# Optimization experiments

Measured on AMD Instinct MI355X. Metric: run time of the kernel, lower is better.

## Reference

```python
import jax, jax.numpy as jnp
import numpy as np

HEADS = 16
LN_EPS = 1e-12
MINUS_INF = -10000.0  # matches DeepSpeed's minus_inf constant


def setup_inputs() -> dict:
    key = jax.random.key(0)
    ks = jax.random.split(key, 6)
    B, S, H = 2, 2048, 2048
    x = jax.random.normal(ks[0], (B, S, H), dtype=jnp.float32)
    mask = jnp.zeros((B, 1, 1, S), dtype=jnp.float32)  # additive float mask (no padding)
    qkvw = jax.random.normal(ks[1], (H, 3 * H), dtype=jnp.float32) * 0.02
    qkvb = jax.random.normal(ks[2], (3 * H,), dtype=jnp.float32) * 0.02
    ow = jax.random.normal(ks[3], (H, H), dtype=jnp.float32) * 0.02
    norm_w = jnp.ones((H,), dtype=jnp.float32)
    norm_b = jnp.zeros((H,), dtype=jnp.float32)
    return {"x": x, "mask": mask, "qkvw": qkvw, "qkvb": qkvb, "ow": ow,
            "norm_w": norm_w, "norm_b": norm_b}


def _layernorm(x, g, b):
    mu = jnp.mean(x, axis=-1, keepdims=True)
    var = jnp.mean(jnp.square(x - mu), axis=-1, keepdims=True)
    return (x - mu) * jax.lax.rsqrt(var + LN_EPS) * g + b


def reference(x, mask, qkvw, qkvb, ow, norm_w, norm_b):
    B, S, H = x.shape
    dh = H // HEADS
    # QKVGemmOp: fused layernorm + QKV projection
    inp_norm = _layernorm(x, norm_w, norm_b)                      # [B,S,H]
    qkv = jnp.einsum('bsh,he->bse', inp_norm, qkvw) + qkvb        # [B,S,3H]
    q, k, v = jnp.split(qkv, 3, axis=-1)
    q = q.reshape(B, S, HEADS, dh).transpose(0, 2, 1, 3)          # [B,Hd,S,dh]
    k = k.reshape(B, S, HEADS, dh).transpose(0, 2, 1, 3)
    v = v.reshape(B, S, HEADS, dh).transpose(0, 2, 1, 3)
    # SoftmaxContextOp: kernel scales q and k each by 1/norm_factor,
    # norm_factor = d_head**0.25 (use_mup=False) -> net scale 1/sqrt(d_head)
    scale = 1.0 / jnp.sqrt(jnp.asarray(dh, dtype=x.dtype))
    scores = jnp.einsum('bhqd,bhkd->bhqk', q, k) * scale          # [B,Hd,S,S]
    causal = jnp.tril(jnp.ones((S, S), dtype=bool))
    scores = jnp.where(causal[None, None], scores + mask, MINUS_INF)
    probs = jax.nn.softmax(scores, axis=-1)
    ctx = jnp.einsum('bhqk,bhkd->bhqd', probs, v)                 # [B,Hd,S,dh]
    ctx = ctx.transpose(0, 2, 1, 3).reshape(B, S, H)
    # VectorMatMulOp: output projection (no bias here)
    out = jnp.einsum('bsh,ho->bso', ctx, ow)                      # [B,S,H]
    return (out, k, v, ctx, inp_norm)
```

## Files before the change

kernel.cpp:

```cpp
#include <hip/hip_runtime.h>

typedef short bf16x8 __attribute__((ext_vector_type(8)));
typedef float floatx4 __attribute__((ext_vector_type(4)));

#define MFMA16(a, b, c) __builtin_amdgcn_mfma_f32_16x16x32_bf16((a), (b), (c), 0, 0, 0)

__device__ __forceinline__ unsigned short f2bf(float f) {
    union { float f; unsigned int u; } v; v.f = f;
    unsigned int u = v.u;
    return (unsigned short)((u + 0x7FFFu + ((u >> 16) & 1u)) >> 16);
}

__device__ __forceinline__ void gld_lds16(const void* g, void* l) {
    __builtin_amdgcn_global_load_lds(
        (const __attribute__((address_space(1))) unsigned int*)g,
        (__attribute__((address_space(3))) unsigned int*)l, 16, 0, 0);
}

__global__ __launch_bounds__(256) void ln_kernel(
        const float* __restrict__ x, const float* __restrict__ g,
        const float* __restrict__ be, float* __restrict__ yo,
        unsigned short* __restrict__ yb) {
    int row = blockIdx.x, t = threadIdx.x;
    const float* xr = x + (size_t)row * 2048;
    float4 a = ((const float4*)xr)[2 * t];
    float4 b = ((const float4*)xr)[2 * t + 1];
    float s = a.x + a.y + a.z + a.w + b.x + b.y + b.z + b.w;
    float q = a.x * a.x + a.y * a.y + a.z * a.z + a.w * a.w +
              b.x * b.x + b.y * b.y + b.z * b.z + b.w * b.w;
    for (int m = 1; m < 64; m <<= 1) { s += __shfl_xor(s, m); q += __shfl_xor(q, m); }
    __shared__ float red[8];
    if ((t & 63) == 0) { red[t >> 6] = s; red[4 + (t >> 6)] = q; }
    __syncthreads();
    s = red[0] + red[1] + red[2] + red[3];
    q = red[4] + red[5] + red[6] + red[7];
    float mean = s * (1.0f / 2048.0f);
    float var = q * (1.0f / 2048.0f) - mean * mean;
    float rs = rsqrtf(var + 1e-12f);
    float4 g0 = ((const float4*)g)[2 * t], g1 = ((const float4*)g)[2 * t + 1];
    float4 b0 = ((const float4*)be)[2 * t], b1 = ((const float4*)be)[2 * t + 1];
    float4 y0, y1;
    y0.x = (a.x - mean) * rs * g0.x + b0.x;
    y0.y = (a.y - mean) * rs * g0.y + b0.y;
    y0.z = (a.z - mean) * rs * g0.z + b0.z;
    y0.w = (a.w - mean) * rs * g0.w + b0.w;
    y1.x = (b.x - mean) * rs * g1.x + b1.x;
    y1.y = (b.y - mean) * rs * g1.y + b1.y;
    y1.z = (b.z - mean) * rs * g1.z + b1.z;
    y1.w = (b.w - mean) * rs * g1.w + b1.w;
    float* yr = yo + (size_t)row * 2048;
    ((float4*)yr)[2 * t] = y0;
    ((float4*)yr)[2 * t + 1] = y1;
    union { unsigned short u[8]; uint4 v; } pk;
    pk.u[0] = f2bf(y0.x); pk.u[1] = f2bf(y0.y); pk.u[2] = f2bf(y0.z); pk.u[3] = f2bf(y0.w);
    pk.u[4] = f2bf(y1.x); pk.u[5] = f2bf(y1.y); pk.u[6] = f2bf(y1.z); pk.u[7] = f2bf(y1.w);
    *(uint4*)(yb + (size_t)row * 2048 + t * 8) = pk.v;
}

__global__ __launch_bounds__(256) void transpose_cvt(
        const float* __restrict__ src, unsigned short* __restrict__ dst,
        int K, int N) {
    __shared__ unsigned short tile[64][73];
    int n0 = blockIdx.x * 64, k0 = blockIdx.y * 64;
    size_t bo = (size_t)blockIdx.z * K * N;
    int t = threadIdx.x;
    for (int p = 0; p < 4; p++) {
        int idx = p * 256 + t; int r = idx >> 4; int c = (idx & 15) * 4;
        float4 v = *(const float4*)(src + bo + (size_t)(k0 + r) * N + n0 + c);
        tile[r][c] = f2bf(v.x); tile[r][c + 1] = f2bf(v.y);
        tile[r][c + 2] = f2bf(v.z); tile[r][c + 3] = f2bf(v.w);
    }
    __syncthreads();
    for (int p = 0; p < 4; p++) {
        int idx = p * 256 + t; int n = idx >> 4; int c = (idx & 15) * 4;
        ushort4 o;
        o.x = tile[c][n]; o.y = tile[c + 1][n];
        o.z = tile[c + 2][n]; o.w = tile[c + 3][n];
        *(ushort4*)(dst + bo + (size_t)(n0 + n) * K + k0 + c) = o;
    }
}

#define NT_QKV 32

__device__ __forceinline__ void stage_A(const unsigned short* __restrict__ Ag,
        unsigned short* As, int mh, int m0, int kt, int tid) {
#pragma unroll
    for (int j = 0; j < 2; j++) {
        int G = j * 512 + tid;
        int s = (G >> 3) & 63;
        int gr = G & 7;
        int row = j * 128 + mh * 64 + s;
        const unsigned short* src =
            Ag + (size_t)(m0 + row) * 2048 + kt * 64 + ((gr ^ (s & 7)) << 3);
        unsigned short* dst = As + j * 8192 + mh * 4096 + (tid >> 6) * 512;
        gld_lds16(src, dst);
    }
}

__device__ __forceinline__ void stage_B(const unsigned short* __restrict__ Bg,
        unsigned short* Bs, int nh, int n0, int kt, int tid) {
#pragma unroll
    for (int j = 0; j < 2; j++) {
        int G = j * 512 + tid;
        int wcc = G >> 8;
        int s = (G >> 3) & 31;
        int gr = G & 7;
        int row = wcc * 64 + nh * 32 + s;
        const unsigned short* src =
            Bg + (size_t)(n0 + row) * 2048 + kt * 64 + ((gr ^ (s & 7)) << 3);
        unsigned short* dst = Bs + wcc * 4096 + nh * 2048 + ((tid >> 6) & 3) * 512;
        gld_lds16(src, dst);
    }
}

__device__ __forceinline__ bf16x8 ldfrag(const unsigned short* S, int row, int ks,
                                         int quad, int ln15) {
    int gr = ((ks << 2) | quad) ^ (ln15 & 7);
    return *(const bf16x8*)(S + row * 64 + gr * 8);
}

__device__ __forceinline__ void qkv_tile(
        const unsigned short* __restrict__ Ag, const unsigned short* __restrict__ Bg,
        unsigned short* Asc, unsigned short* Bsc,
        unsigned short* Asn, unsigned short* Bsn,
        int t, int m0, int n0, int tid, int wr, int wc, int ln15, int quad,
        floatx4 (&acc)[8][4]) {
    bf16x8 a[4][2], bb[2][2];
#pragma unroll
    for (int m = 0; m < 4; m++) {
        a[m][0] = ldfrag(Asc, wr * 128 + m * 16 + ln15, 0, quad, ln15);
        a[m][1] = ldfrag(Asc, wr * 128 + m * 16 + ln15, 1, quad, ln15);
    }
#pragma unroll
    for (int n = 0; n < 2; n++) {
        bb[n][0] = ldfrag(Bsc, wc * 64 + n * 16 + ln15, 0, quad, ln15);
        bb[n][1] = ldfrag(Bsc, wc * 64 + n * 16 + ln15, 1, quad, ln15);
    }
    if (t + 1 < NT_QKV) stage_B(Bg, Bsn, 0, n0, t + 1, tid);
    __builtin_amdgcn_s_barrier();
    asm volatile("s_waitcnt lgkmcnt(0)" ::: "memory");
    __builtin_amdgcn_sched_barrier(0);
    __builtin_amdgcn_s_setprio(1);
#pragma unroll
    for (int m = 0; m < 4; m++)
#pragma unroll
        for (int n = 0; n < 2; n++) {
            acc[m][n] = MFMA16(a[m][0], bb[n][0], acc[m][n]);
            acc[m][n] = MFMA16(a[m][1], bb[n][1], acc[m][n]);
        }
    __builtin_amdgcn_s_setprio(0);
    __builtin_amdgcn_s_barrier();
#pragma unroll
    for (int n = 0; n < 2; n++) {
        bb[n][0] = ldfrag(Bsc, wc * 64 + (2 + n) * 16 + ln15, 0, quad, ln15);
        bb[n][1] = ldfrag(Bsc, wc * 64 + (2 + n) * 16 + ln15, 1, quad, ln15);
    }
    if (t + 2 < NT_QKV) stage_A(Ag, Asc, 0, m0, t + 2, tid);
    __builtin_amdgcn_s_barrier();
    asm volatile("s_waitcnt lgkmcnt(0)" ::: "memory");
    __builtin_amdgcn_sched_barrier(0);
    __builtin_amdgcn_s_setprio(1);
#pragma unroll
    for (int m = 0; m < 4; m++)
#pragma unroll
        for (int n = 0; n < 2; n++) {
            acc[m][2 + n] = MFMA16(a[m][0], bb[n][0], acc[m][2 + n]);
            acc[m][2 + n] = MFMA16(a[m][1], bb[n][1], acc[m][2 + n]);
        }
    __builtin_amdgcn_s_setprio(0);
    __builtin_amdgcn_s_barrier();
#pragma unroll
    for (int m = 0; m < 4; m++) {
        a[m][0] = ldfrag(Asc, wr * 128 + (4 + m) * 16 + ln15, 0, quad, ln15);
        a[m][1] = ldfrag(Asc, wr * 128 + (4 + m) * 16 + ln15, 1, quad, ln15);
    }
    if (t + 2 < NT_QKV) stage_B(Bg, Bsc, 1, n0, t + 2, tid);
    __builtin_amdgcn_s_barrier();
    asm volatile("s_waitcnt lgkmcnt(0)" ::: "memory");
    __builtin_amdgcn_sched_barrier(0);
    __builtin_amdgcn_s_setprio(1);
#pragma unroll
    for (int m = 0; m < 4; m++)
#pragma unroll
        for (int n = 0; n < 2; n++) {
            acc[4 + m][2 + n] = MFMA16(a[m][0], bb[n][0], acc[4 + m][2 + n]);
            acc[4 + m][2 + n] = MFMA16(a[m][1], bb[n][1], acc[4 + m][2 + n]);
        }
    __builtin_amdgcn_s_setprio(0);
    __builtin_amdgcn_s_barrier();
#pragma unroll
    for (int n = 0; n < 2; n++) {
        bb[n][0] = ldfrag(Bsc, wc * 64 + n * 16 + ln15, 0, quad, ln15);
        bb[n][1] = ldfrag(Bsc, wc * 64 + n * 16 + ln15, 1, quad, ln15);
    }
    if (t + 2 < NT_QKV) stage_A(Ag, Asc, 1, m0, t + 2, tid);
    __builtin_amdgcn_s_barrier();
    asm volatile("s_waitcnt lgkmcnt(0)" ::: "memory");
    __builtin_amdgcn_sched_barrier(0);
    __builtin_amdgcn_s_setprio(1);
#pragma unroll
    for (int m = 0; m < 4; m++)
#pragma unroll
        for (int n = 0; n < 2; n++) {
            acc[4 + m][n] = MFMA16(a[m][0], bb[n][0], acc[4 + m][n]);
            acc[4 + m][n] = MFMA16(a[m][1], bb[n][1], acc[4 + m][n]);
        }
    __builtin_amdgcn_s_setprio(0);
    if (t + 2 < NT_QKV) asm volatile("s_waitcnt vmcnt(6)" ::: "memory");
    else                asm volatile("s_waitcnt vmcnt(0)" ::: "memory");
    __builtin_amdgcn_s_barrier();
}

__global__ __launch_bounds__(512, 2) void gemm_qkv(
        const unsigned short* __restrict__ A, const unsigned short* __restrict__ Bt,
        const float* __restrict__ bias, float* __restrict__ ko,
        float* __restrict__ vo, unsigned short* __restrict__ qws,
        unsigned short* __restrict__ kbf) {
    __shared__ __align__(16) unsigned short As[2][16384];
    __shared__ __align__(16) unsigned short Bs[2][16384];
    int bid = blockIdx.x;
    int wg = (bid & 7) * 48 + (bid >> 3);
    int mt = wg / 24, ntile = wg % 24;
    int m0 = mt * 256, n0 = ntile * 256;
    int tid = threadIdx.x;
    int wave = tid >> 6, lane = tid & 63, ln15 = lane & 15, quad = lane >> 4;
    int wr = wave >> 2, wc = wave & 3;
    floatx4 acc[8][4] = {};
    stage_B(Bt, Bs[0], 0, n0, 0, tid);
    stage_A(A, As[0], 0, m0, 0, tid);
    stage_B(Bt, Bs[0], 1, n0, 0, tid);
    stage_A(A, As[0], 1, m0, 0, tid);
    stage_A(A, As[1], 0, m0, 1, tid);
    stage_B(Bt, Bs[1], 1, n0, 1, tid);
    stage_A(A, As[1], 1, m0, 1, tid);
    asm volatile("s_waitcnt vmcnt(6)" ::: "memory");
    __builtin_amdgcn_s_barrier();
#pragma unroll 1
    for (int t = 0; t < NT_QKV; t += 2) {
        qkv_tile(A, Bt, As[0], Bs[0], As[1], Bs[1], t,     m0, n0, tid, wr, wc, ln15, quad, acc);
        qkv_tile(A, Bt, As[1], Bs[1], As[0], Bs[0], t + 1, m0, n0, tid, wr, wc, ln15, quad, acc);
    }
#pragma unroll
    for (int mi = 0; mi < 8; mi++) {
        int row = m0 + wr * 128 + mi * 16 + quad * 4;
#pragma unroll
        for (int ni = 0; ni < 4; ni++) {
            int col = n0 + wc * 64 + ni * 16 + ln15;
            float bv = bias[col];
#pragma unroll
            for (int r = 0; r < 4; r++) {
                float val = acc[mi][ni][r] + bv;
                int rr = row + r;
                int b = rr >> 11, s = rr & 2047;
                if (col < 2048) {
                    qws[(size_t)rr * 2048 + col] = f2bf(val);
                } else if (col < 4096) {
                    int cc = col - 2048; int h = cc >> 7, d = cc & 127;
                    size_t o = ((size_t)(b * 16 + h) * 2048 + s) * 128 + d;
                    ko[o] = val;
                    kbf[o] = f2bf(val);
                } else {
                    int cc = col - 4096; int h = cc >> 7, d = cc & 127;
                    vo[((size_t)(b * 16 + h) * 2048 + s) * 128 + d] = val;
                }
            }
        }
    }
}

__global__ __launch_bounds__(256) void gemm_out(
        const float* __restrict__ Actx, const unsigned short* __restrict__ Bt,
        float* __restrict__ out) {
    __shared__ unsigned short As[128 * 72];
    __shared__ unsigned short Bs[128 * 72];
    int m0 = blockIdx.y * 128, n0 = blockIdx.x * 128;
    int t = threadIdx.x;
    int wave = t >> 6, lane = t & 63, ln15 = lane & 15, quad = lane >> 4;
    int wm = wave >> 1, wn = wave & 1;
    floatx4 acc[4][4] = {};
    for (int k0 = 0; k0 < 2048; k0 += 64) {
        for (int p = 0; p < 4; p++) {
            int idx = p * 256 + t; int r = idx >> 3; int c = (idx & 7) * 8;
            const float* ap = Actx + (size_t)(m0 + r) * 2048 + k0 + c;
            float4 u0 = ((const float4*)ap)[0], u1 = ((const float4*)ap)[1];
            union { unsigned short u[8]; uint4 v; } pk;
            pk.u[0] = f2bf(u0.x); pk.u[1] = f2bf(u0.y); pk.u[2] = f2bf(u0.z); pk.u[3] = f2bf(u0.w);
            pk.u[4] = f2bf(u1.x); pk.u[5] = f2bf(u1.y); pk.u[6] = f2bf(u1.z); pk.u[7] = f2bf(u1.w);
            *(uint4*)&As[r * 72 + c] = pk.v;
            *(uint4*)&Bs[r * 72 + c] = *(const uint4*)(Bt + (size_t)(n0 + r) * 2048 + k0 + c);
        }
        __syncthreads();
        for (int ks = 0; ks < 2; ks++) {
            bf16x8 af[4], bfr[4];
            for (int i = 0; i < 4; i++)
                af[i] = *(const bf16x8*)&As[(wm * 64 + i * 16 + ln15) * 72 + ks * 32 + quad * 8];
            for (int i = 0; i < 4; i++)
                bfr[i] = *(const bf16x8*)&Bs[(wn * 64 + i * 16 + ln15) * 72 + ks * 32 + quad * 8];
            for (int mi = 0; mi < 4; mi++)
                for (int ni = 0; ni < 4; ni++)
                    acc[mi][ni] = MFMA16(af[mi], bfr[ni], acc[mi][ni]);
        }
        __syncthreads();
    }
    for (int mi = 0; mi < 4; mi++) {
        int row = m0 + wm * 64 + mi * 16 + quad * 4;
        for (int ni = 0; ni < 4; ni++) {
            int col = n0 + wn * 64 + ni * 16 + ln15;
            for (int r = 0; r < 4; r++)
                out[(size_t)(row + r) * 2048 + col] = acc[mi][ni][r];
        }
    }
}

__global__ __launch_bounds__(256) void attn_kernel(
        const unsigned short* __restrict__ qws, const unsigned short* __restrict__ kbf,
        const unsigned short* __restrict__ vT, const float* __restrict__ mask,
        float* __restrict__ ctxo) {
    __shared__ unsigned short Ks[64 * 136];
    __shared__ unsigned short Vt[128 * 72];
    __shared__ unsigned short Pl[4 * 16 * 72];
    int jp = blockIdx.x, h = blockIdx.y, b = blockIdx.z;
    int t = threadIdx.x, wave = t >> 6, lane = t & 63, ln15 = lane & 15, quad = lane >> 4;
    const float scale = 0.08838834764831845f;

    const unsigned short* kb = kbf + (size_t)(b * 16 + h) * 2048 * 128;
    const unsigned short* vTb = vT + (size_t)(b * 16 + h) * 128 * 2048;
    const float* mb = mask + (size_t)b * 2048;

    for (int half = 0; half < 2; half++) {
        int qt = half ? (31 - jp) : jp;
        int Q0 = qt * 64;

        bf16x8 qf[4];
        const unsigned short* qbase =
            qws + ((size_t)(b * 2048 + Q0 + wave * 16 + ln15)) * 2048 + h * 128;
        for (int ks = 0; ks < 4; ks++)
            qf[ks] = *(const bf16x8*)(qbase + ks * 32 + quad * 8);

        float m_r[4], l_r[4];
        floatx4 o[8] = {};
        for (int r = 0; r < 4; r++) { m_r[r] = -1e30f; l_r[r] = 0.0f; }

        int nkt = qt + 1;
        for (int kt = 0; kt < nkt; kt++) {
            int c0 = kt * 64;
            for (int p = 0; p < 4; p++) {
                int idx = p * 256 + t; int r = idx >> 4; int c = (idx & 15) * 8;
                *(uint4*)&Ks[r * 136 + c] = *(const uint4*)(kb + (size_t)(c0 + r) * 128 + c);
            }
            for (int p = 0; p < 4; p++) {
                int idx = p * 256 + t; int d = idx >> 3; int sg = (idx & 7) * 8;
                *(uint4*)&Vt[d * 72 + sg] = *(const uint4*)(vTb + (size_t)d * 2048 + c0 + sg);
            }
            __syncthreads();

            floatx4 cs[4] = {};
            for (int ks = 0; ks < 4; ks++)
                for (int ni = 0; ni < 4; ni++) {
                    bf16x8 kfr = *(const bf16x8*)&Ks[(ni * 16 + ln15) * 136 + ks * 32 + quad * 8];
                    cs[ni] = MFMA16(qf[ks], kfr, cs[ni]);
                }

            float sv[4][4];
            float mt[4] = {-1e30f, -1e30f, -1e30f, -1e30f};
            if (kt == qt) {
                for (int ni = 0; ni < 4; ni++) {
                    int cg = c0 + ni * 16 + ln15;
                    float mk = mb[cg];
                    for (int r = 0; r < 4; r++) {
                        int qg = Q0 + wave * 16 + quad * 4 + r;
                        float v = (cg <= qg) ? cs[ni][r] * scale + mk : -10000.0f;
                        sv[ni][r] = v;
                        mt[r] = fmaxf(mt[r], v);
                    }
                }
            } else {
                for (int ni = 0; ni < 4; ni++) {
                    float mk = mb[c0 + ni * 16 + ln15];
                    for (int r = 0; r < 4; r++) {
                        float v = cs[ni][r] * scale + mk;
                        sv[ni][r] = v;
                        mt[r] = fmaxf(mt[r], v);
                    }
                }
            }
            for (int m = 1; m < 16; m <<= 1)
                for (int r = 0; r < 4; r++) mt[r] = fmaxf(mt[r], __shfl_xor(mt[r], m));
            float alpha[4], lt[4];
            for (int r = 0; r < 4; r++) {
                float mn = fmaxf(m_r[r], mt[r]);
                alpha[r] = __expf(m_r[r] - mn);
                m_r[r] = mn;
                lt[r] = 0.0f;
            }
            for (int ni = 0; ni < 4; ni++)
                for (int r = 0; r < 4; r++) {
                    float p = __expf(sv[ni][r] - m_r[r]);
                    sv[ni][r] = p;
                    lt[r] += p;
                }
            for (int m = 1; m < 16; m <<= 1)
                for (int r = 0; r < 4; r++) lt[r] += __shfl_xor(lt[r], m);
            for (int r = 0; r < 4; r++) l_r[r] = l_r[r] * alpha[r] + lt[r];
            for (int nj = 0; nj < 8; nj++)
                for (int r = 0; r < 4; r++) o[nj][r] *= alpha[r];

            unsigned short* pw = &Pl[wave * 16 * 72];
            for (int ni = 0; ni < 4; ni++)
                for (int r = 0; r < 4; r++)
                    pw[(quad * 4 + r) * 72 + ni * 16 + ln15] = f2bf(sv[ni][r]);

            for (int ks2 = 0; ks2 < 2; ks2++) {
                bf16x8 pf = *(const bf16x8*)&Pl[(wave * 16 + ln15) * 72 + ks2 * 32 + quad * 8];
                for (int nj = 0; nj < 8; nj++) {
                    bf16x8 vf = *(const bf16x8*)&Vt[(nj * 16 + ln15) * 72 + ks2 * 32 + quad * 8];
                    o[nj] = MFMA16(pf, vf, o[nj]);
                }
            }
            __syncthreads();
        }

        float rl[4];
        for (int r = 0; r < 4; r++) rl[r] = 1.0f / l_r[r];
        for (int nj = 0; nj < 8; nj++)
            for (int r = 0; r < 4; r++) {
                int s = Q0 + wave * 16 + quad * 4 + r;
                ctxo[((size_t)(b * 2048 + s)) * 2048 + h * 128 + nj * 16 + ln15] = o[nj][r] * rl[r];
            }
    }
}

extern "C" void kernel_launch(void* const* d_in, const int* in_sizes, int n_in,
                              void* d_out, int out_size, void* d_ws, size_t ws_size,
                              hipStream_t stream) {
    const float* x      = (const float*)d_in[0];
    const float* mask   = (const float*)d_in[1];
    const float* qkvw   = (const float*)d_in[2];
    const float* qkvb   = (const float*)d_in[3];
    const float* ow     = (const float*)d_in[4];
    const float* norm_w = (const float*)d_in[5];
    const float* norm_b = (const float*)d_in[6];

    float* out      = (float*)d_out;
    float* k_out    = out + 8388608;
    float* v_out    = out + 16777216;
    float* ctx_out  = out + 25165824;
    float* norm_out = out + 33554432;

    unsigned short* ws    = (unsigned short*)d_ws;
    unsigned short* xn    = ws;
    unsigned short* qkvwT = ws + 8388608;
    unsigned short* owT   = ws + 8388608 + 12582912;
    unsigned short* qws   = owT + 4194304;
    unsigned short* vT    = qws + 8388608;
    unsigned short* kbf   = vT + 8388608;

    ln_kernel<<<4096, 256, 0, stream>>>(x, norm_w, norm_b, norm_out, xn);
    transpose_cvt<<<dim3(96, 32, 1), 256, 0, stream>>>(qkvw, qkvwT, 2048, 6144);
    transpose_cvt<<<dim3(32, 32, 1), 256, 0, stream>>>(ow, owT, 2048, 2048);
    gemm_qkv<<<dim3(384), 512, 0, stream>>>(xn, qkvwT, qkvb, k_out, v_out, qws, kbf);
    transpose_cvt<<<dim3(2, 32, 32), 256, 0, stream>>>(v_out, vT, 2048, 128);
    attn_kernel<<<dim3(16, 16, 2), 256, 0, stream>>>(qws, kbf, vT, mask, ctx_out);
    gemm_out<<<dim3(16, 32), 256, 0, stream>>>(ctx_out, owT, out);
}
```

Before: 543.9 us.

## Restructure QKV GEMM prefetch to one-tile double buffering and remap tiles per XCD

The QKV GEMM prologue now stages only the first K-tile. Inside the loop, each phase prefetches the next tile's A and B halves into the alternate LDS buffer, instead of loading two tiles ahead into the current buffer. Every phase now ends with a uniform vmcnt(4) wait plus barrier, wrapped in new sync macros. The block-to-tile mapping is also changed so each XCD works on a contiguous 4x12 region of M×N tiles, aiming for better L2 reuse of A and B. The shallower prefetch depth and the extra vmcnt waits per phase may expose more global-load latency.

```diff
diff --git a/kernel.cpp b/kernel.cpp
--- a/kernel.cpp
+++ b/kernel.cpp
@@ -119,6 +119,17 @@
     return *(const bf16x8*)(S + row * 64 + gr * 8);
 }
 
+#define PHASE_SYNC()                                        \
+    __builtin_amdgcn_s_barrier();                           \
+    asm volatile("s_waitcnt lgkmcnt(0)" ::: "memory");      \
+    __builtin_amdgcn_sched_barrier(0);                      \
+    __builtin_amdgcn_s_setprio(1)
+
+#define PHASE_END()                                         \
+    __builtin_amdgcn_s_setprio(0);                          \
+    asm volatile("s_waitcnt vmcnt(4)" ::: "memory");        \
+    __builtin_amdgcn_s_barrier()
+
 __device__ __forceinline__ void qkv_tile(
         const unsigned short* __restrict__ Ag, const unsigned short* __restrict__ Bg,
         unsigned short* Asc, unsigned short* Bsc,
@@ -126,6 +137,7 @@
         int t, int m0, int n0, int tid, int wr, int wc, int ln15, int quad,
         floatx4 (&acc)[8][4]) {
     bf16x8 a[4][2], bb[2][2];
+    bool pf = (t + 1 < NT_QKV);
 #pragma unroll
     for (int m = 0; m < 4; m++) {
         a[m][0] = ldfrag(Asc, wr * 128 + m * 16 + ln15, 0, quad, ln15);
@@ -136,11 +148,8 @@
         bb[n][0] = ldfrag(Bsc, wc * 64 + n * 16 + ln15, 0, quad, ln15);
         bb[n][1] = ldfrag(Bsc, wc * 64 + n * 16 + ln15, 1, quad, ln15);
     }
-    if (t + 1 < NT_QKV) stage_B(Bg, Bsn, 0, n0, t + 1, tid);
-    __builtin_amdgcn_s_barrier();
-    asm volatile("s_waitcnt lgkmcnt(0)" ::: "memory");
-    __builtin_amdgcn_sched_barrier(0);
-    __builtin_amdgcn_s_setprio(1);
+    if (pf) stage_B(Bg, Bsn, 0, n0, t + 1, tid);
+    PHASE_SYNC();
 #pragma unroll
     for (int m = 0; m < 4; m++)
 #pragma unroll
@@ -148,18 +157,14 @@
             acc[m][n] = MFMA16(a[m][0], bb[n][0], acc[m][n]);
             acc[m][n] = MFMA16(a[m][1], bb[n][1], acc[m][n]);
         }
-    __builtin_amdgcn_s_setprio(0);
-    __builtin_amdgcn_s_barrier();
+    PHASE_END();
 #pragma unroll
     for (int n = 0; n < 2; n++) {
         bb[n][0] = ldfrag(Bsc, wc * 64 + (2 + n) * 16 + ln15, 0, quad, ln15);
         bb[n][1] = ldfrag(Bsc, wc * 64 + (2 + n) * 16 + ln15, 1, quad, ln15);
     }
-    if (t + 2 < NT_QKV) stage_A(Ag, Asc, 0, m0, t + 2, tid);
-    __builtin_amdgcn_s_barrier();
-    asm volatile("s_waitcnt lgkmcnt(0)" ::: "memory");
-    __builtin_amdgcn_sched_barrier(0);
-    __builtin_amdgcn_s_setprio(1);
+    if (pf) stage_A(Ag, Asn, 0, m0, t + 1, tid);
+    PHASE_SYNC();
 #pragma unroll
     for (int m = 0; m < 4; m++)
 #pragma unroll
@@ -167,18 +172,14 @@
             acc[m][2 + n] = MFMA16(a[m][0], bb[n][0], acc[m][2 + n]);
             acc[m][2 + n] = MFMA16(a[m][1], bb[n][1], acc[m][2 + n]);
         }
-    __builtin_amdgcn_s_setprio(0);
-    __builtin_amdgcn_s_barrier();
+    PHASE_END();
 #pragma unroll
     for (int m = 0; m < 4; m++) {
         a[m][0] = ldfrag(Asc, wr * 128 + (4 + m) * 16 + ln15, 0, quad, ln15);
         a[m][1] = ldfrag(Asc, wr * 128 + (4 + m) * 16 + ln15, 1, quad, ln15);
     }
-    if (t + 2 < NT_QKV) stage_B(Bg, Bsc, 1, n0, t + 2, tid);
-    __builtin_amdgcn_s_barrier();
-    asm volatile("s_waitcnt lgkmcnt(0)" ::: "memory");
-    __builtin_amdgcn_sched_barrier(0);
-    __builtin_amdgcn_s_setprio(1);
+    if (pf) stage_B(Bg, Bsn, 1, n0, t + 1, tid);
+    PHASE_SYNC();
 #pragma unroll
     for (int m = 0; m < 4; m++)
 #pragma unroll
@@ -186,18 +187,14 @@
             acc[4 + m][2 + n] = MFMA16(a[m][0], bb[n][0], acc[4 + m][2 + n]);
             acc[4 + m][2 + n] = MFMA16(a[m][1], bb[n][1], acc[4 + m][2 + n]);
         }
-    __builtin_amdgcn_s_setprio(0);
-    __builtin_amdgcn_s_barrier();
+    PHASE_END();
 #pragma unroll
     for (int n = 0; n < 2; n++) {
         bb[n][0] = ldfrag(Bsc, wc * 64 + n * 16 + ln15, 0, quad, ln15);
         bb[n][1] = ldfrag(Bsc, wc * 64 + n * 16 + ln15, 1, quad, ln15);
     }
-    if (t + 2 < NT_QKV) stage_A(Ag, Asc, 1, m0, t + 2, tid);
-    __builtin_amdgcn_s_barrier();
-    asm volatile("s_waitcnt lgkmcnt(0)" ::: "memory");
-    __builtin_amdgcn_sched_barrier(0);
-    __builtin_amdgcn_s_setprio(1);
+    if (pf) stage_A(Ag, Asn, 1, m0, t + 1, tid);
+    PHASE_SYNC();
 #pragma unroll
     for (int m = 0; m < 4; m++)
 #pragma unroll
@@ -205,10 +202,7 @@
             acc[4 + m][n] = MFMA16(a[m][0], bb[n][0], acc[4 + m][n]);
             acc[4 + m][n] = MFMA16(a[m][1], bb[n][1], acc[4 + m][n]);
         }
-    __builtin_amdgcn_s_setprio(0);
-    if (t + 2 < NT_QKV) asm volatile("s_waitcnt vmcnt(6)" ::: "memory");
-    else                asm volatile("s_waitcnt vmcnt(0)" ::: "memory");
-    __builtin_amdgcn_s_barrier();
+    PHASE_END();
 }
 
 __global__ __launch_bounds__(512, 2) void gemm_qkv(
@@ -219,8 +213,9 @@
     __shared__ __align__(16) unsigned short As[2][16384];
     __shared__ __align__(16) unsigned short Bs[2][16384];
     int bid = blockIdx.x;
-    int wg = (bid & 7) * 48 + (bid >> 3);
-    int mt = wg / 24, ntile = wg % 24;
+    int xcd = bid & 7, idx = bid >> 3;
+    int mt = (xcd & 3) * 4 + idx / 12;
+    int ntile = (xcd >> 2) * 12 + idx % 12;
     int m0 = mt * 256, n0 = ntile * 256;
     int tid = threadIdx.x;
     int wave = tid >> 6, lane = tid & 63, ln15 = lane & 15, quad = lane >> 4;
@@ -230,10 +225,7 @@
     stage_A(A, As[0], 0, m0, 0, tid);
     stage_B(Bt, Bs[0], 1, n0, 0, tid);
     stage_A(A, As[0], 1, m0, 0, tid);
-    stage_A(A, As[1], 0, m0, 1, tid);
-    stage_B(Bt, Bs[1], 1, n0, 1, tid);
-    stage_A(A, As[1], 1, m0, 1, tid);
-    asm volatile("s_waitcnt vmcnt(6)" ::: "memory");
+    asm volatile("s_waitcnt vmcnt(4)" ::: "memory");
     __builtin_amdgcn_s_barrier();
 #pragma unroll 1
     for (int t = 0; t < NT_QKV; t += 2) {
```

New measurement: 551.3 us. About the same (+1.4%).
